# Kernel tuning notes

Measured on AMD Instinct MI355X. Metric: run time of the kernel, lower is better.

The kernel has to match this reference:

```python
import jax, jax.numpy as jnp
import numpy as np

T, B, D_IN = 1024, 64, 17
H_MAIN = 150   # per-direction hidden of main bi-GRU (hidden_dim=300)
H_HIER = 128   # per-direction hidden of hier bi-GRU (hier_hidden=256)
M = 16         # uniform measure length (eoM fires every M steps)
N_MEAS = T // M
N_PITCH, N_KS = 35, 15
PAD_P, PAD_K = 34, 14


def _gru(x, Wih, Whh, bih, bhh):
    # x: [T, N, D]; torch GRU gate order is (r, z, n)
    H = Whh.shape[1]
    gi_all = jnp.einsum('tnd,gd->tng', x, Wih) + bih  # input-side gates, precomputed

    def step(h, gi):
        gh = h @ Whh.T + bhh
        ir, iz, inn = jnp.split(gi, 3, axis=-1)
        hr, hz, hn = jnp.split(gh, 3, axis=-1)
        r = jax.nn.sigmoid(ir + hr)
        z = jax.nn.sigmoid(iz + hz)
        n = jnp.tanh(inn + r * hn)
        h_new = (1.0 - z) * n + z * h
        return h_new, h_new

    h0 = jnp.zeros((x.shape[1], H), x.dtype)
    _, ys = jax.lax.scan(step, h0, gi_all)
    return ys


def _bigru(x, pf, pb):
    yf = _gru(x, *pf)
    yb = _gru(x[::-1], *pb)[::-1]
    return jnp.concatenate([yf, yb], axis=-1)


def _ce(logits, targets, pad_idx):
    # mean cross-entropy with ignore_index=pad_idx
    logp = jax.nn.log_softmax(logits, axis=-1)
    mask = (targets != pad_idx).astype(logits.dtype)
    nll = -jnp.take_along_axis(logp, targets[:, None], axis=1)[:, 0]
    return jnp.sum(nll * mask) / jnp.maximum(jnp.sum(mask), 1.0)


def _forward(sentences, mWih_f, mWhh_f, mbih_f, mbhh_f, mWih_b, mWhh_b, mbih_b, mbhh_b,
             hWih_f, hWhh_f, hbih_f, hbhh_f, hWih_b, hWhh_b, hbih_b, hbhh_b,
             Wq, bq, Wv, bv, Wp, bp, Wk, bk, pitches, keysignatures):
    # main bi-GRU over full sequences: [T, B, 300]
    rnn_out = _bigru(sentences, (mWih_f, mWhh_f, mbih_f, mbhh_f),
                     (mWih_b, mWhh_b, mbih_b, mbhh_b))
    H2 = rnn_out.shape[-1]
    # carve uniform measures: [T,B,H2] -> [M, B*N_MEAS, H2]
    seg = rnn_out.reshape(N_MEAS, M, B, H2).transpose(1, 2, 0, 3).reshape(M, B * N_MEAS, H2)
    hier = _bigru(seg, (hWih_f, hWhh_f, hbih_f, hbhh_f),
                  (hWih_b, hWhh_b, hbih_b, hbhh_b))  # [M, B*N_MEAS, 256]
    HH = hier.shape[-1]
    # attention per measure: query = value = hier outputs [B*N_MEAS, M, 256]
    hv = hier.reshape(M, B, N_MEAS, HH).transpose(1, 2, 0, 3).reshape(B * N_MEAS, M, HH)
    q = hv @ Wq.T + bq
    v = hv @ Wv.T + bv
    attn = jax.nn.softmax(jnp.einsum('nld,nmd->nlm', q, v), axis=-1)
    ctx = jnp.einsum('nlm,nmd->nd', attn, hv).reshape(B, N_MEAS, HH)  # sum over l of attn@value
    # repeat each measure context over its M timesteps: [T, B, 256]
    ctx_t = jnp.repeat(ctx, M, axis=1).transpose(1, 0, 2)
    stacked = jnp.concatenate([rnn_out, ctx_t], axis=-1)  # [T, B, 556]
    out_pitch = stacked @ Wp.T + bp   # [T, B, 35]
    out_ks = ctx_t @ Wk.T + bk        # [T, B, 15]
    return (_ce(out_pitch.reshape(-1, N_PITCH), pitches.reshape(-1), PAD_P)
            + _ce(out_ks.reshape(-1, N_KS), keysignatures.reshape(-1), PAD_K))


def setup_inputs() -> dict:
    key = jax.random.key(0)
    ks = jax.random.split(key, 32)

    def w(i, *shape):
        return jax.random.normal(ks[i], shape, jnp.float32) * 0.05

    G_M, G_H = 3 * H_MAIN, 3 * H_HIER
    inp = {
        'sentences': jax.random.normal(ks[0], (T, B, D_IN), jnp.float32),
        'pitches': jax.random.randint(ks[1], (T, B), 0, PAD_P),
        'keysignatures': jax.random.randint(ks[2], (T, B), 0, PAD_K),
        'sentences_len': jnp.full((B,), T, dtype=jnp.int32),
        'eoM': jnp.tile(((jnp.arange(T) % M) == M - 1).astype(jnp.int32)[:, None], (1, B)),
        'mWih_f': w(3, G_M, D_IN), 'mWhh_f': w(4, G_M, H_MAIN), 'mbih_f': w(5, G_M), 'mbhh_f': w(6, G_M),
        'mWih_b': w(7, G_M, D_IN), 'mWhh_b': w(8, G_M, H_MAIN), 'mbih_b': w(9, G_M), 'mbhh_b': w(10, G_M),
        'hWih_f': w(11, G_H, 2 * H_MAIN), 'hWhh_f': w(12, G_H, H_HIER), 'hbih_f': w(13, G_H), 'hbhh_f': w(14, G_H),
        'hWih_b': w(15, G_H, 2 * H_MAIN), 'hWhh_b': w(16, G_H, H_HIER), 'hbih_b': w(17, G_H), 'hbhh_b': w(18, G_H),
        'Wq': w(19, 2 * H_HIER, 2 * H_HIER), 'bq': w(20, 2 * H_HIER),
        'Wv': w(21, 2 * H_HIER, 2 * H_HIER), 'bv': w(22, 2 * H_HIER),
        'Wp': w(23, N_PITCH, 2 * H_MAIN + 2 * H_HIER), 'bp': w(24, N_PITCH),
        'Wk': w(25, N_KS, 2 * H_HIER), 'bk': w(26, N_KS),
    }
    return inp


def reference(sentences, pitches, keysignatures, sentences_len, eoM,
              mWih_f, mWhh_f, mbih_f, mbhh_f, mWih_b, mWhh_b, mbih_b, mbhh_b,
              hWih_f, hWhh_f, hbih_f, hbhh_f, hWih_b, hWhh_b, hbih_b, hbhh_b,
              Wq, bq, Wv, bv, Wp, bp, Wk, bk):
    # sentences_len/eoM encode the (uniform) measure structure M=16, full lengths;
    # the segment layout is baked in statically, so they are structural constants here.
    return _forward(sentences, mWih_f, mWhh_f, mbih_f, mbhh_f, mWih_b, mWhh_b, mbih_b, mbhh_b,
                    hWih_f, hWhh_f, hbih_f, hbhh_f, hWih_b, hWhh_b, hbih_b, hbhh_b,
                    Wq, bq, Wv, bv, Wp, bp, Wk, bk, pitches, keysignatures)
```

## Files before the change

kernel.cpp:

```cpp
#include <hip/hip_runtime.h>
#include <cstddef>

constexpr int kT   = 1024;
constexpr int kB   = 64;
constexpr int kDIN = 17;
constexpr int kHM  = 150;
constexpr int kHH  = 128;
constexpr int kM   = 16;
constexpr int kD2  = 300;
constexpr int kNP  = 35;
constexpr int kNK  = 15;

constexpr size_t OFF_RNN16  = 0;
constexpr size_t OFF_HV16   = 10485760;
constexpr size_t OFF_HSAVE  = 18874368;
constexpr size_t OFF_PTPACK = 19988480;
constexpr size_t OFF_U      = 20021248;
constexpr size_t OFF_W      = 20021504;
constexpr size_t OFF_C0     = 20021760;
constexpr size_t OFF_ACC    = 20021776;
constexpr size_t OFF_KSLOGP = 20021792;
constexpr size_t OFF_CLOG   = 20083232;
constexpr size_t OFF_BPACK  = 20318752;
constexpr size_t OFF_BPACKL = 20490784;

typedef __bf16 bf16x8 __attribute__((ext_vector_type(8)));
typedef float f32x4 __attribute__((ext_vector_type(4)));

__device__ __forceinline__ unsigned short f2bf(float f) {
  unsigned u = __float_as_uint(f);
  u += 0x7FFFu + ((u >> 16) & 1u);
  return (unsigned short)(u >> 16);
}
__device__ __forceinline__ float bf2f(unsigned short v) {
  return __uint_as_float(((unsigned)v) << 16);
}
__device__ __forceinline__ float sigm(float x) {
  return __builtin_amdgcn_rcpf(1.f + __expf(-x));
}
__device__ __forceinline__ float tanh_fast(float x) {
  return 1.f - 2.f * __builtin_amdgcn_rcpf(__expf(2.f * x) + 1.f);
}

__global__ __launch_bounds__(640, 2) void k_mega(
    const float* __restrict__ x,
    const float* __restrict__ mWih_f, const float* __restrict__ mWhh_f,
    const float* __restrict__ mWih_b, const float* __restrict__ mWhh_b,
    const float* __restrict__ mbih_f, const float* __restrict__ mbhh_f,
    const float* __restrict__ mbih_b, const float* __restrict__ mbhh_b,
    const float* __restrict__ hWih_f, const float* __restrict__ hWhh_f,
    const float* __restrict__ hWih_b, const float* __restrict__ hWhh_b,
    const float* __restrict__ Wp,
    const float* __restrict__ Wq, const float* __restrict__ bq,
    const float* __restrict__ Wv, const float* __restrict__ bv,
    unsigned short* __restrict__ rnn16,
    unsigned short* __restrict__ bpack,
    unsigned short* __restrict__ bpackL,
    unsigned short* __restrict__ pp,
    float* __restrict__ u, float* __restrict__ w,
    float* __restrict__ c0, float* __restrict__ acc,
    float* __restrict__ hsave,
    int t_begin, int t_end)
{
  __shared__ __align__(16) unsigned short hx[2][160];
  __shared__ __align__(16) unsigned short hist[2][16][160];
  __shared__ __align__(16) unsigned short xall[kT][32];
  const int blk = blockIdx.x;
  if (blk < 128) {
    const int d = blk & 1, b = blk >> 1;
    const int tid = threadIdx.x, wv = tid >> 6, lane = tid & 63;
    const int col = lane & 15, q8 = (lane >> 4) * 8;
    for (int i = tid; i < 2 * 160; i += 640) ((unsigned short*)hx)[i] = 0;
    for (int i = tid; i < 2 * 16 * 160; i += 640) ((unsigned short*)hist)[i] = 0;
    {
      const int rlo = d ? (kT - t_end) : t_begin;
      for (int i = tid; i < 512 * 32; i += 640) {
        const int tt = rlo + (i >> 5), c = i & 31;
        xall[tt][c] = (c < kDIN) ? f2bf(x[((size_t)tt * kB + b) * kDIN + c])
                                 : (unsigned short)0;
      }
    }
    const float* bih = d ? mbih_b : mbih_f;
    const float* bhh = d ? mbhh_b : mbhh_f;
    const float* Wihd = d ? mWih_b : mWih_f;
    const float* Whhd = d ? mWhh_b : mWhh_f;
    const int j = wv * 16 + col;
    const bool actv = (lane < 16) && (j < kHM);
    float br = 0.f, bz = 0.f, bnx = 0.f, bnh = 0.f;
    if (actv) {
      br  = bih[j] + bhh[j];
      bz  = bih[150 + j] + bhh[150 + j];
      bnx = bih[300 + j];
      bnh = bhh[300 + j];
    }
    bf16x8 bw[3][6];
    const int gts[3] = { wv, 10 + wv, 20 + wv };
    const int kb = (lane >> 4) * 8;
#pragma unroll
    for (int gi = 0; gi < 3; gi++) {
      const int slot = gts[gi] * 16 + col;
      const int type = slot / 160, jh = slot - type * 160;
      const int row = type * 150 + jh;
      const bool valid = (jh < 150);
#pragma unroll
      for (int kt = 0; kt < 6; kt++) {
        union { bf16x8 v; unsigned short us[8]; } tmp;
        if (kt < 5) {
          const int k0 = kt * 32 + kb;
          if (valid && (k0 + 8 <= 150)) {
#pragma unroll
            for (int p = 0; p < 4; p++) {
              const float2 f2 = *(const float2*)&Whhd[row * 150 + k0 + 2 * p];
              tmp.us[2 * p]     = f2bf(f2.x);
              tmp.us[2 * p + 1] = f2bf(f2.y);
            }
          } else {
#pragma unroll
            for (int jj = 0; jj < 8; jj++) {
              const int k = k0 + jj;
              tmp.us[jj] = (valid && k < 150) ? f2bf(Whhd[row * 150 + k])
                                              : (unsigned short)0;
            }
          }
        } else {
#pragma unroll
          for (int jj = 0; jj < 8; jj++) {
            const int k = kb + jj;
            tmp.us[jj] = (valid && k < 17) ? f2bf(Wihd[row * 17 + k])
                                           : (unsigned short)0;
          }
        }
        bw[gi][kt] = tmp.v;
      }
    }
    float h_old = 0.f;
    if (t_begin > 0 && actv) {
      h_old = hsave[blk * 160 + j];
      hx[t_begin & 1][j] = f2bf(h_old);
    }
    __syncthreads();

    for (int t = t_begin; t < t_end; t++) {
      const int tx = d ? (kT - 1 - t) : t;
      const int buf = t & 1;
      bf16x8 afr[6];
#pragma unroll
      for (int kt = 0; kt < 5; kt++) afr[kt] = *(const bf16x8*)&hx[buf][kt * 32 + q8];
      afr[5] = *(const bf16x8*)&xall[tx][q8];
      f32x4 aR0 = (f32x4)(0.f), aR1 = (f32x4)(0.f);
      f32x4 aZ0 = (f32x4)(0.f), aZ1 = (f32x4)(0.f);
      f32x4 aN0 = (f32x4)(0.f), aN1 = (f32x4)(0.f);
      f32x4 aX  = (f32x4)(0.f);
#pragma unroll
      for (int kt = 0; kt < 6; kt++) {
        const bf16x8 af = afr[kt];
        if ((kt & 1) == 0) {
          aR0 = __builtin_amdgcn_mfma_f32_16x16x32_bf16(af, bw[0][kt], aR0, 0, 0, 0);
          aZ0 = __builtin_amdgcn_mfma_f32_16x16x32_bf16(af, bw[1][kt], aZ0, 0, 0, 0);
          aN0 = __builtin_amdgcn_mfma_f32_16x16x32_bf16(af, bw[2][kt], aN0, 0, 0, 0);
        } else if (kt < 5) {
          aR1 = __builtin_amdgcn_mfma_f32_16x16x32_bf16(af, bw[0][kt], aR1, 0, 0, 0);
          aZ1 = __builtin_amdgcn_mfma_f32_16x16x32_bf16(af, bw[1][kt], aZ1, 0, 0, 0);
          aN1 = __builtin_amdgcn_mfma_f32_16x16x32_bf16(af, bw[2][kt], aN1, 0, 0, 0);
        } else {
          aR1 = __builtin_amdgcn_mfma_f32_16x16x32_bf16(af, bw[0][5], aR1, 0, 0, 0);
          aZ1 = __builtin_amdgcn_mfma_f32_16x16x32_bf16(af, bw[1][5], aZ1, 0, 0, 0);
          aX  = __builtin_amdgcn_mfma_f32_16x16x32_bf16(af, bw[2][5], aX, 0, 0, 0);
        }
      }
      if (actv) {
        const float r = sigm(aR0[0] + aR1[0] + br);
        const float z = sigm(aZ0[0] + aZ1[0] + bz);
        const float n = tanh_fast(aX[0] + bnx + r * (aN0[0] + aN1[0] + bnh));
        h_old = (1.f - z) * n + z * h_old;
        const unsigned short us = f2bf(h_old);
        hx[buf ^ 1][j] = us;
        hist[(t >> 4) & 1][t & 15][j] = us;
      }
      __syncthreads();
      if ((t & 15) == 15) {
        const int hb = (t >> 4) & 1;
        const int toff = tid / 40, ch = tid - toff * 40;
        const int tg = t - 15 + toff;
        const int txg = d ? (kT - 1 - tg) : tg;
        *(ushort4*)&rnn16[((size_t)txg * kB + b) * 320 + d * 160 + ch * 4] =
            *(const ushort4*)&hist[hb][toff][ch * 4];
      }
    }
    if (t_end < kT && actv) hsave[blk * 160 + j] = h_old;
  } else if (blk < 199) {
    const int sub = threadIdx.x >> 6, lane = threadIdx.x & 63;
    int bid = (blk - 128) * 10 + sub;
    if (bid >= 702) return;
    if (bid < 672) {
      const int kt = bid % 14;
      const int nt = (bid / 14) % 24;
      const int d  = bid / (14 * 24);
      const float* Wih = d ? hWih_b : hWih_f;
      const float* Whh = d ? hWhh_b : hWhh_f;
      const int n = nt * 16 + (lane & 15);
      const int kbase = kt * 32 + (lane >> 4) * 8;
      unsigned short* dst = bpack + ((((size_t)d * 24 + nt) * 14 + kt) * 64 + lane) * 8;
#pragma unroll
      for (int jj = 0; jj < 8; jj++) {
        const int k = kbase + jj;
        float f = 0.f;
        if (kt < 10) {
          if (k < 150) f = Wih[n * 300 + k];
          else if (k >= 160 && k < 310) f = Wih[n * 300 + (k - 10)];
        } else {
          f = Whh[n * 128 + (k - 320)];
        }
        dst[jj] = f2bf(f);
      }
    } else {
      bid -= 672;
      const int kt = bid % 10, nt = bid / 10;
      const int n = nt * 16 + (lane & 15);
      const int kbase = kt * 32 + (lane >> 4) * 8;
      unsigned short* dst = bpackL + (((size_t)bid) * 64 + lane) * 8;
#pragma unroll
      for (int jj = 0; jj < 8; jj++) {
        const int k = kbase + jj;
        float f = 0.f;
        if (n < kNP) {
          if (k < 150) f = Wp[n * 556 + k];
          else if (k >= 160 && k < 310) f = Wp[n * 556 + (k - 10)];
        }
        dst[jj] = f2bf(f);
      }
    }
  } else if (blk < 212) {
    const int sub = threadIdx.x >> 6, lane = threadIdx.x & 63;
    const int bid = (blk - 199) * 10 + sub;
    if (bid >= 128) return;
    const int kt = bid & 7, nt = bid >> 3;
    const int c = nt * 16 + (lane & 15);
    const int e0 = kt * 32 + (lane >> 4) * 8;
    float av[8];
#pragma unroll
    for (int jj = 0; jj < 8; jj++) av[jj] = 0.f;
    for (int a = 0; a < 256; a++) {
      const float wq = Wq[a * 256 + c];
#pragma unroll
      for (int jj = 0; jj < 8; jj++) av[jj] += wq * Wv[a * 256 + e0 + jj];
    }
    unsigned short* dst = pp + ((size_t)bid * 64 + lane) * 8;
#pragma unroll
    for (int jj = 0; jj < 8; jj++) dst[jj] = f2bf(av[jj]);
  } else {
    const int a = threadIdx.x;
    if (a >= 256) return;
    float us = 0.f, ws = 0.f;
    for (int jj = 0; jj < 256; jj++) {
      us += Wq[jj * 256 + a] * bv[jj];
      ws += bq[jj] * Wv[jj * 256 + a];
    }
    u[a] = us; w[a] = ws;
    if (a == 0) {
      float cc = 0.f;
      for (int jj = 0; jj < 256; jj++) cc += bq[jj] * bv[jj];
      c0[0] = cc;
      acc[0] = acc[1] = acc[2] = acc[3] = acc[4] = 0.f;
    }
  }
}

__global__ __launch_bounds__(512, 1) void k_hier_mfma(
    const unsigned short* __restrict__ rnn16,
    const unsigned short* __restrict__ bpack,
    const float* __restrict__ bihf, const float* __restrict__ bhhf,
    const float* __restrict__ bihb, const float* __restrict__ bhhb,
    unsigned short* __restrict__ hv16)
{
  const int d = blockIdx.x & 1;
  const int bn0 = (blockIdx.x >> 1) * 16;
  const int tid = threadIdx.x;
  const int w = tid >> 6;
  const int lane = tid & 63;
  const int q = lane >> 4, col = lane & 15, q8 = q * 8;

  __shared__ __align__(16) unsigned short x_s[2][16][328];
  __shared__ __align__(16) unsigned short h_s[16][136];

  for (int i = tid; i < 16 * 136; i += 512) ((unsigned short*)h_s)[i] = 0;
  const float* bih = d ? bihb : bihf;
  const float* bhh = d ? bhhb : bhhf;
  const int j = w * 16 + col;
  const float biR  = bih[j] + bhh[j];
  const float biZ  = bih[128 + j] + bhh[128 + j];
  const float biNX = bih[256 + j];
  const float biNH = bhh[256 + j];
  float h32r[4] = {0.f, 0.f, 0.f, 0.f};

  bf16x8 bw[3][14];
  const unsigned short* bpd = bpack + (size_t)d * 24 * 14 * 64 * 8;
  const int nts[3] = { w, 8 + w, 16 + w };
#pragma unroll
  for (int gi = 0; gi < 3; gi++)
#pragma unroll
    for (int kt = 0; kt < 14; kt++)
      bw[gi][kt] = *(const bf16x8*)&bpd[(((size_t)nts[gi] * 14 + kt) * 64 + lane) * 8];

  const int i0 = tid,        r0 = i0 / 40, c0 = i0 - r0 * 40;
  const int i1 = tid + 512,  r1 = i1 / 40, c1 = i1 - r1 * 40;
  const int bnA = bn0 + r0, bbA = bnA >> 6, nnA = bnA & 63;
  const int bnB = bn0 + r1, bbB = bnB >> 6, nnB = bnB & 63;

  {
    const int mx0 = d ? 15 : 0;
    *(uint4*)&x_s[0][r0][c0 * 8] =
        *(const uint4*)&rnn16[((size_t)(nnA * 16 + mx0) * 64 + bbA) * 320 + c0 * 8];
    if (tid < 128)
      *(uint4*)&x_s[0][r1][c1 * 8] =
          *(const uint4*)&rnn16[((size_t)(nnB * 16 + mx0) * 64 + bbB) * 320 + c1 * 8];
  }
  __syncthreads();

  for (int m = 0; m < kM; m++) {
    const int mx = d ? (15 - m) : m;
    const int buf = m & 1;
    uint4 pf0, pf1;
    const bool has = (m + 1 < kM);
    if (has) {
      const int mxn = d ? (15 - (m + 1)) : (m + 1);
      pf0 = *(const uint4*)&rnn16[((size_t)(nnA * 16 + mxn) * 64 + bbA) * 320 + c0 * 8];
      if (tid < 128)
        pf1 = *(const uint4*)&rnn16[((size_t)(nnB * 16 + mxn) * 64 + bbB) * 320 + c1 * 8];
    }
    f32x4 aR = (f32x4)(0.f), aZ = (f32x4)(0.f), aNX = (f32x4)(0.f), aNH = (f32x4)(0.f);
#pragma unroll
    for (int kt = 0; kt < 14; kt++) {
      const bf16x8 af = (kt < 10) ? *(const bf16x8*)&x_s[buf][col][kt * 32 + q8]
                                  : *(const bf16x8*)&h_s[col][(kt - 10) * 32 + q8];
      aR = __builtin_amdgcn_mfma_f32_16x16x32_bf16(af, bw[0][kt], aR, 0, 0, 0);
      aZ = __builtin_amdgcn_mfma_f32_16x16x32_bf16(af, bw[1][kt], aZ, 0, 0, 0);
      if (kt < 10) aNX = __builtin_amdgcn_mfma_f32_16x16x32_bf16(af, bw[2][kt], aNX, 0, 0, 0);
      else         aNH = __builtin_amdgcn_mfma_f32_16x16x32_bf16(af, bw[2][kt], aNH, 0, 0, 0);
    }
    __syncthreads();
#pragma unroll
    for (int i = 0; i < 4; i++) {
      const int row = q * 4 + i;
      const float rr = sigm(aR[i] + biR);
      const float zz = sigm(aZ[i] + biZ);
      const float nn2 = tanh_fast(aNX[i] + biNX + rr * (aNH[i] + biNH));
      const float hnew = (1.f - zz) * nn2 + zz * h32r[i];
      h32r[i] = hnew;
      const unsigned short us = f2bf(hnew);
      h_s[row][j] = us;
      hv16[((size_t)(bn0 + row) * kM + mx) * 256 + d * kHH + j] = us;
    }
    if (has) {
      *(uint4*)&x_s[buf ^ 1][r0][c0 * 8] = pf0;
      if (tid < 128) *(uint4*)&x_s[buf ^ 1][r1][c1 * 8] = pf1;
    }
    __syncthreads();
  }
}

__global__ __launch_bounds__(256) void k_attn_ctx(
    const unsigned short* __restrict__ hv16, const unsigned short* __restrict__ ptpack,
    const float* __restrict__ u, const float* __restrict__ w,
    const float* __restrict__ c0p,
    const float* __restrict__ Wp, const float* __restrict__ bp,
    const float* __restrict__ Wk, const float* __restrict__ bk,
    float* __restrict__ clog, float* __restrict__ kslogp) {
  const int tid = threadIdx.x;
  const int wv = tid >> 6, lane = tid & 63, col = lane & 15, q = lane >> 4, q8 = q * 8;
  __shared__ __align__(16) unsigned short hv16s[16][264];
  __shared__ __align__(16) unsigned short Ts16[16][264];
  __shared__ __align__(16) float W2[50][260];
  __shared__ __align__(16) float cs[256];
  __shared__ __align__(16) float us[256], wss[256];
  __shared__ float pu[16][17], pw[16][17];
  __shared__ float uh[16], wh[16], SM[16];
  __shared__ float As[16][17];
  __shared__ float arr[64];
  __shared__ float bps[35], bks[15];
  const float c0 = c0p[0];
  for (int i = tid; i < 35 * 256; i += 256) { const int r = i >> 8, c = i & 255; W2[r][c] = Wp[r * 556 + 300 + c]; }
  for (int i = tid; i < 15 * 256; i += 256) { const int r = i >> 8, c = i & 255; W2[35 + r][c] = Wk[r * 256 + c]; }
  us[tid] = u[tid];
  wss[tid] = w[tid];
  if (tid < 35) bps[tid] = bp[tid];
  else if (tid < 50) bks[tid - 35] = bk[tid - 35];
  bf16x8 bpt[4][8];
#pragma unroll
  for (int i2 = 0; i2 < 4; i2++)
#pragma unroll
    for (int kt = 0; kt < 8; kt++)
      bpt[i2][kt] = *(const bf16x8*)&ptpack[((((size_t)(wv * 4 + i2)) * 8 + kt) * 64 + lane) * 8];

  const int srow = tid >> 4, sci = (tid & 15) * 16;
  {
    const unsigned short* src = hv16 + (size_t)(blockIdx.x * 8) * 4096;
#pragma unroll
    for (int k = 0; k < 16; k += 4)
      *(ushort4*)&hv16s[srow][sci + k] = *(const ushort4*)&src[srow * 256 + sci + k];
  }
  __syncthreads();

  for (int ni = 0; ni < 8; ni++) {
    const int n = blockIdx.x * 8 + ni;
    ushort4 pf[4];
    if (ni + 1 < 8) {
      const unsigned short* src = hv16 + (size_t)(n + 1) * 4096;
#pragma unroll
      for (int k2 = 0; k2 < 4; k2++) pf[k2] = *(const ushort4*)&src[srow * 256 + sci + k2 * 4];
    }
    {
      f32x4 acc4[4];
#pragma unroll
      for (int i2 = 0; i2 < 4; i2++) acc4[i2] = (f32x4)(0.f);
#pragma unroll
      for (int kt = 0; kt < 8; kt++) {
        const bf16x8 af = *(const bf16x8*)&hv16s[col][kt * 32 + q8];
#pragma unroll
        for (int i2 = 0; i2 < 4; i2++)
          acc4[i2] = __builtin_amdgcn_mfma_f32_16x16x32_bf16(af, bpt[i2][kt], acc4[i2], 0, 0, 0);
      }
#pragma unroll
      for (int i2 = 0; i2 < 4; i2++) {
        const int nt = wv * 4 + i2;
#pragma unroll
        for (int i = 0; i < 4; i++) Ts16[q * 4 + i][nt * 16 + col] = f2bf(acc4[i2][i]);
      }
    }
    {
      const int l = tid >> 4, s = tid & 15;
      float su = 0.f, sw = 0.f;
#pragma unroll
      for (int a0 = 0; a0 < 16; a0++) {
        const int a = s * 16 + a0;
        const float hvv = bf2f(hv16s[l][a]);
        su += hvv * us[a];
        sw += hvv * wss[a];
      }
      pu[l][s] = su; pw[l][s] = sw;
    }
    __syncthreads();
    if (tid < 16) { float s2 = 0.f; for (int s = 0; s < 16; s++) s2 += pu[tid][s]; uh[tid] = s2; }
    else if (tid < 32) { float s2 = 0.f; for (int s = 0; s < 16; s++) s2 += pw[tid - 16][s]; wh[tid - 16] = s2; }
    __syncthreads();
    if (tid < 64) {
      f32x4 sa = (f32x4)(0.f);
#pragma unroll
      for (int kt = 0; kt < 8; kt++) {
        const bf16x8 af  = *(const bf16x8*)&hv16s[col][kt * 32 + q8];
        const bf16x8 bts = *(const bf16x8*)&Ts16[col][kt * 32 + q8];
        sa = __builtin_amdgcn_mfma_f32_16x16x32_bf16(af, bts, sa, 0, 0, 0);
      }
#pragma unroll
      for (int i = 0; i < 4; i++) {
        const int l = q * 4 + i;
        float sc = sa[i] + c0 + uh[l] + wh[col];
        float mxv = sc;
#pragma unroll
        for (int o = 8; o >= 1; o >>= 1) mxv = fmaxf(mxv, __shfl_xor(mxv, o, 16));
        const float e = __expf(sc - mxv);
        float se = e;
#pragma unroll
        for (int o = 8; o >= 1; o >>= 1) se += __shfl_xor(se, o, 16);
        As[l][col] = e / se;
      }
    }
    __syncthreads();
    if (tid < 16) {
      float s = 0.f;
      for (int l2 = 0; l2 < 16; l2++) s += As[l2][tid];
      SM[tid] = s;
    }
    __syncthreads();
    {
      float cv = 0.f;
#pragma unroll
      for (int m2 = 0; m2 < 16; m2++) cv += SM[m2] * bf2f(hv16s[m2][tid]);
      cs[tid] = cv;
    }
    __syncthreads();
    if (ni + 1 < 8) {
#pragma unroll
      for (int k2 = 0; k2 < 4; k2++) *(ushort4*)&hv16s[srow][sci + k2 * 4] = pf[k2];
    }
    {
      const int o = tid >> 2, s = tid & 3;
      float v = 0.f;
      if (o < 50) {
        for (int k0 = 0; k0 < 64; k0 += 4) {
          const int k = s * 64 + k0;
          const float4 wq = *(const float4*)&W2[o][k];
          const float4 cq = *(const float4*)&cs[k];
          v += wq.x * cq.x + wq.y * cq.y + wq.z * cq.z + wq.w * cq.w;
        }
      }
      v += __shfl_xor(v, 1);
      v += __shfl_xor(v, 2);
      if (o < 50 && s == 0) arr[o] = v;
    }
    __syncthreads();
    if (tid < 35) clog[n * kNP + tid] = arr[tid] + bps[tid];
    if (tid >= 64 && tid < 80) {
      const int t2 = tid - 64;
      float kk = (t2 < 15) ? arr[35 + t2] + bks[t2] : -1e30f;
      float mxv = kk;
#pragma unroll
      for (int off = 8; off >= 1; off >>= 1) mxv = fmaxf(mxv, __shfl_xor(mxv, off, 16));
      const float e = (t2 < 15) ? __expf(kk - mxv) : 0.f;
      float se = e;
#pragma unroll
      for (int off = 8; off >= 1; off >>= 1) se += __shfl_xor(se, off, 16);
      if (t2 < 15) kslogp[n * kNK + t2] = kk - mxv - __logf(se);
    }
    __syncthreads();
  }
}

__global__ __launch_bounds__(256, 2) void k_loss_mfma(
    const unsigned short* __restrict__ rnn16,
    const unsigned short* __restrict__ bpackL,
    const float* __restrict__ clog,
    const float* __restrict__ ks_logp,
    const int* __restrict__ pitches, const int* __restrict__ kss,
    float* __restrict__ acc, float* __restrict__ out) {
  const int tid = threadIdx.x, w = tid >> 6, lane = tid & 63;
  const int col = lane & 15, q = lane >> 4, q8 = q * 8;
  bf16x8 bl[3][10];
#pragma unroll
  for (int nt = 0; nt < 3; nt++)
#pragma unroll
    for (int kt = 0; kt < 10; kt++)
      bl[nt][kt] = *(const bf16x8*)&bpackL[(((size_t)nt * 10 + kt) * 64 + lane) * 8];

  float sp = 0.f, cp = 0.f, sk = 0.f, ck = 0.f;
#pragma unroll
  for (int mt = 0; mt < 2; mt++) {
    const int rowbase = blockIdx.x * 128 + w * 32 + mt * 16;
    f32x4 a0 = (f32x4)(0.f), a1 = (f32x4)(0.f), a2 = (f32x4)(0.f);
#pragma unroll
    for (int kt = 0; kt < 10; kt++) {
      const bf16x8 af = *(const bf16x8*)&rnn16[(size_t)(rowbase + col) * 320 + kt * 32 + q8];
      a0 = __builtin_amdgcn_mfma_f32_16x16x32_bf16(af, bl[0][kt], a0, 0, 0, 0);
      a1 = __builtin_amdgcn_mfma_f32_16x16x32_bf16(af, bl[1][kt], a1, 0, 0, 0);
      a2 = __builtin_amdgcn_mfma_f32_16x16x32_bf16(af, bl[2][kt], a2, 0, 0, 0);
    }
#pragma unroll
    for (int i = 0; i < 4; i++) {
      const int row = rowbase + q * 4 + i;
      const int t = row >> 6, b = row & 63;
      const int bn = b * 64 + (t >> 4);
      const float lg0 = a0[i] + clog[bn * kNP + col];
      const float lg1 = a1[i] + clog[bn * kNP + 16 + col];
      const float lg2 = (col < 3) ? (a2[i] + clog[bn * kNP + 32 + col]) : -1e30f;
      float mx = fmaxf(fmaxf(lg0, lg1), lg2);
#pragma unroll
      for (int o = 8; o >= 1; o >>= 1) mx = fmaxf(mx, __shfl_xor(mx, o, 16));
      float se = __expf(lg0 - mx) + __expf(lg1 - mx) + __expf(lg2 - mx);
#pragma unroll
      for (int o = 8; o >= 1; o >>= 1) se += __shfl_xor(se, o, 16);
      const int tp = pitches[row];
      const float cand = (tp < 16) ? a0[i] : (tp < 32) ? a1[i] : a2[i];
      const float tva = __shfl(cand, (lane & 48) | (tp & 15), 64);
      if (col == 0 && tp != 34) {
        sp += (mx + __logf(se)) - (tva + clog[bn * kNP + tp]);
        cp += 1.f;
      }
      if (col == 1) {
        const int tk = kss[row];
        if (tk != 14) { sk -= ks_logp[bn * kNK + tk]; ck += 1.f; }
      }
    }
  }
#pragma unroll
  for (int o = 32; o >= 1; o >>= 1) {
    sp += __shfl_xor(sp, o, 64);
    cp += __shfl_xor(cp, o, 64);
    sk += __shfl_xor(sk, o, 64);
    ck += __shfl_xor(ck, o, 64);
  }
  if (lane == 0) {
    atomicAdd(&acc[0], sp); atomicAdd(&acc[1], cp);
    atomicAdd(&acc[2], sk); atomicAdd(&acc[3], ck);
  }
  __syncthreads();
  if (tid == 0) {
    __threadfence();
    const float done = atomicAdd(&acc[4], 1.f);
    if (done == (float)(gridDim.x - 1)) {
      const float a0 = atomicAdd(&acc[0], 0.f);
      const float a1 = atomicAdd(&acc[1], 0.f);
      const float a2 = atomicAdd(&acc[2], 0.f);
      const float a3 = atomicAdd(&acc[3], 0.f);
      out[0] = a0 / fmaxf(a1, 1.f) + a2 / fmaxf(a3, 1.f);
    }
  }
}

extern "C" void kernel_launch(void* const* d_in, const int* in_sizes, int n_in,
                              void* d_out, int out_size, void* d_ws, size_t ws_size,
                              hipStream_t stream) {
  (void)in_sizes; (void)n_in; (void)out_size; (void)ws_size;
  const float* sent    = (const float*)d_in[0];
  const int*   pitches = (const int*)d_in[1];
  const int*   kss     = (const int*)d_in[2];
  const float* mWih_f  = (const float*)d_in[5];
  const float* mWhh_f  = (const float*)d_in[6];
  const float* mbih_f  = (const float*)d_in[7];
  const float* mbhh_f  = (const float*)d_in[8];
  const float* mWih_b  = (const float*)d_in[9];
  const float* mWhh_b  = (const float*)d_in[10];
  const float* mbih_b  = (const float*)d_in[11];
  const float* mbhh_b  = (const float*)d_in[12];
  const float* hWih_f  = (const float*)d_in[13];
  const float* hWhh_f  = (const float*)d_in[14];
  const float* hbih_f  = (const float*)d_in[15];
  const float* hbhh_f  = (const float*)d_in[16];
  const float* hWih_b  = (const float*)d_in[17];
  const float* hWhh_b  = (const float*)d_in[18];
  const float* hbih_b  = (const float*)d_in[19];
  const float* hbhh_b  = (const float*)d_in[20];
  const float* Wq      = (const float*)d_in[21];
  const float* bq      = (const float*)d_in[22];
  const float* Wv      = (const float*)d_in[23];
  const float* bv      = (const float*)d_in[24];
  const float* Wp      = (const float*)d_in[25];
  const float* bp      = (const float*)d_in[26];
  const float* Wk      = (const float*)d_in[27];
  const float* bk      = (const float*)d_in[28];
  float* ws  = (float*)d_ws;
  float* out = (float*)d_out;
  unsigned short* rnn16  = (unsigned short*)(ws + OFF_RNN16);
  unsigned short* hv16   = (unsigned short*)(ws + OFF_HV16);
  unsigned short* ptpack = (unsigned short*)(ws + OFF_PTPACK);
  unsigned short* bpackL = (unsigned short*)(ws + OFF_BPACKL);
  unsigned short* bpack  = (unsigned short*)(ws + OFF_BPACK);
  float* hsave = ws + OFF_HSAVE;

  k_mega<<<213, 640, 0, stream>>>(sent,
                                  mWih_f, mWhh_f, mWih_b, mWhh_b,
                                  mbih_f, mbhh_f, mbih_b, mbhh_b,
                                  hWih_f, hWhh_f, hWih_b, hWhh_b, Wp,
                                  Wq, bq, Wv, bv,
                                  rnn16, bpack, bpackL, ptpack,
                                  ws + OFF_U, ws + OFF_W, ws + OFF_C0, ws + OFF_ACC,
                                  hsave, 0, 512);
  k_mega<<<128, 640, 0, stream>>>(sent,
                                  mWih_f, mWhh_f, mWih_b, mWhh_b,
                                  mbih_f, mbhh_f, mbih_b, mbhh_b,
                                  hWih_f, hWhh_f, hWih_b, hWhh_b, Wp,
                                  Wq, bq, Wv, bv,
                                  rnn16, bpack, bpackL, ptpack,
                                  ws + OFF_U, ws + OFF_W, ws + OFF_C0, ws + OFF_ACC,
                                  hsave, 512, 1024);
  k_hier_mfma<<<512, 512, 0, stream>>>(rnn16, bpack,
                                       hbih_f, hbhh_f, hbih_b, hbhh_b, hv16);
  k_attn_ctx<<<512, 256, 0, stream>>>(hv16, ptpack, ws + OFF_U, ws + OFF_W,
                                      ws + OFF_C0, Wp, bp, Wk, bk,
                                      ws + OFF_CLOG, ws + OFF_KSLOGP);
  k_loss_mfma<<<512, 256, 0, stream>>>(rnn16, bpackL, ws + OFF_CLOG, ws + OFF_KSLOGP,
                                       pitches, kss, ws + OFF_ACC, out);
}
```

Measured before the change: 1.026 ms.

## Split main GRU into four phases and stage loss inputs in LDS

The main bi-GRU recurrence now runs as four kernel launches of 256 steps each instead of two of 512. The per-block input tile in shared memory shrinks from 1024 to 256 rows, which cuts LDS use in k_mega and may let more blocks or waves share a CU. Separately, the loss kernel now covers 64 rows per block instead of 128. Each block first copies its rnn16 rows into padded shared memory with 16-byte loads and then feeds the MFMAs from LDS, replacing strided global loads. The cost is two extra launches with hidden-state save and restore, plus an extra sync and LDS traffic in the loss kernel; the remaining unseen part of the loss kernel must also work with the new row mapping.

```diff
diff --git a/kernel.cpp b/kernel.cpp
--- a/kernel.cpp
+++ b/kernel.cpp
@@ -64,7 +64,7 @@
 {
   __shared__ __align__(16) unsigned short hx[2][160];
   __shared__ __align__(16) unsigned short hist[2][16][160];
-  __shared__ __align__(16) unsigned short xall[kT][32];
+  __shared__ __align__(16) unsigned short xall[256][32];
   const int blk = blockIdx.x;
   if (blk < 128) {
     const int d = blk & 1, b = blk >> 1;
@@ -72,13 +72,11 @@
     const int col = lane & 15, q8 = (lane >> 4) * 8;
     for (int i = tid; i < 2 * 160; i += 640) ((unsigned short*)hx)[i] = 0;
     for (int i = tid; i < 2 * 16 * 160; i += 640) ((unsigned short*)hist)[i] = 0;
-    {
-      const int rlo = d ? (kT - t_end) : t_begin;
-      for (int i = tid; i < 512 * 32; i += 640) {
-        const int tt = rlo + (i >> 5), c = i & 31;
-        xall[tt][c] = (c < kDIN) ? f2bf(x[((size_t)tt * kB + b) * kDIN + c])
-                                 : (unsigned short)0;
-      }
+    const int rlo = d ? (kT - t_end) : t_begin;
+    for (int i = tid; i < 256 * 32; i += 640) {
+      const int tt = rlo + (i >> 5), c = i & 31;
+      xall[i >> 5][c] = (c < kDIN) ? f2bf(x[((size_t)tt * kB + b) * kDIN + c])
+                                   : (unsigned short)0;
     }
     const float* bih = d ? mbih_b : mbih_f;
     const float* bhh = d ? mbhh_b : mbhh_f;
@@ -146,7 +144,7 @@
       bf16x8 afr[6];
 #pragma unroll
       for (int kt = 0; kt < 5; kt++) afr[kt] = *(const bf16x8*)&hx[buf][kt * 32 + q8];
-      afr[5] = *(const bf16x8*)&xall[tx][q8];
+      afr[5] = *(const bf16x8*)&xall[tx - rlo][q8];
       f32x4 aR0 = (f32x4)(0.f), aR1 = (f32x4)(0.f);
       f32x4 aZ0 = (f32x4)(0.f), aZ1 = (f32x4)(0.f);
       f32x4 aN0 = (f32x4)(0.f), aN1 = (f32x4)(0.f);
@@ -525,6 +523,7 @@
     float* __restrict__ acc, float* __restrict__ out) {
   const int tid = threadIdx.x, w = tid >> 6, lane = tid & 63;
   const int col = lane & 15, q = lane >> 4, q8 = q * 8;
+  __shared__ __align__(16) unsigned short xls[64][328];
   bf16x8 bl[3][10];
 #pragma unroll
   for (int nt = 0; nt < 3; nt++)
@@ -532,14 +531,22 @@
     for (int kt = 0; kt < 10; kt++)
       bl[nt][kt] = *(const bf16x8*)&bpackL[(((size_t)nt * 10 + kt) * 64 + lane) * 8];
 
+  {
+    const size_t base = (size_t)blockIdx.x * 64;
+    for (int i = tid; i < 64 * 40; i += 256) {
+      const int r = i / 40, c = i - r * 40;
+      *(uint4*)&xls[r][c * 8] = *(const uint4*)&rnn16[(base + r) * 320 + c * 8];
+    }
+  }
+  __syncthreads();
+
   float sp = 0.f, cp = 0.f, sk = 0.f, ck = 0.f;
-#pragma unroll
-  for (int mt = 0; mt < 2; mt++) {
-    const int rowbase = blockIdx.x * 128 + w * 32 + mt * 16;
+  {
+    const int rowbase = blockIdx.x * 64 + w * 16;
     f32x4 a0 = (f32x4)(0.f), a1 = (f32x4)(0.f), a2 = (f32x4)(0.f);
 #pragma unroll
     for (int kt = 0; kt < 10; kt++) {
-      const bf16x8 af = *(const bf16x8*)&rnn16[(size_t)(rowbase + col) * 320 + kt * 32 + q8];
+      const bf16x8 af = *(const bf16x8*)&xls[w * 16 + col][kt * 32 + q8];
       a0 = __builtin_amdgcn_mfma_f32_16x16x32_bf16(af, bl[0][kt], a0, 0, 0, 0);
       a1 = __builtin_amdgcn_mfma_f32_16x16x32_bf16(af, bl[1][kt], a1, 0, 0, 0);
       a2 = __builtin_amdgcn_mfma_f32_16x16x32_bf16(af, bl[2][kt], a2, 0, 0, 0);
@@ -636,27 +643,22 @@
   unsigned short* bpack  = (unsigned short*)(ws + OFF_BPACK);
   float* hsave = ws + OFF_HSAVE;
 
-  k_mega<<<213, 640, 0, stream>>>(sent,
-                                  mWih_f, mWhh_f, mWih_b, mWhh_b,
-                                  mbih_f, mbhh_f, mbih_b, mbhh_b,
-                                  hWih_f, hWhh_f, hWih_b, hWhh_b, Wp,
-                                  Wq, bq, Wv, bv,
-                                  rnn16, bpack, bpackL, ptpack,
-                                  ws + OFF_U, ws + OFF_W, ws + OFF_C0, ws + OFF_ACC,
-                                  hsave, 0, 512);
-  k_mega<<<128, 640, 0, stream>>>(sent,
-                                  mWih_f, mWhh_f, mWih_b, mWhh_b,
-                                  mbih_f, mbhh_f, mbih_b, mbhh_b,
-                                  hWih_f, hWhh_f, hWih_b, hWhh_b, Wp,
-                                  Wq, bq, Wv, bv,
-                                  rnn16, bpack, bpackL, ptpack,
-                                  ws + OFF_U, ws + OFF_W, ws + OFF_C0, ws + OFF_ACC,
-                                  hsave, 512, 1024);
+  for (int ph = 0; ph < 4; ph++) {
+    const int grid = (ph == 0) ? 213 : 128;
+    k_mega<<<grid, 640, 0, stream>>>(sent,
+                                     mWih_f, mWhh_f, mWih_b, mWhh_b,
+                                     mbih_f, mbhh_f, mbih_b, mbhh_b,
+                                     hWih_f, hWhh_f, hWih_b, hWhh_b, Wp,
+                                     Wq, bq, Wv, bv,
+                                     rnn16, bpack, bpackL, ptpack,
+                                     ws + OFF_U, ws + OFF_W, ws + OFF_C0, ws + OFF_ACC,
+                                     hsave, ph * 256, (ph + 1) * 256);
+  }
   k_hier_mfma<<<512, 512, 0, stream>>>(rnn16, bpack,
                                        hbih_f, hbhh_f, hbih_b, hbhh_b, hv16);
   k_attn_ctx<<<512, 256, 0, stream>>>(hv16, ptpack, ws + OFF_U, ws + OFF_W,
                                       ws + OFF_C0, Wp, bp, Wk, bk,
                                       ws + OFF_CLOG, ws + OFF_KSLOGP);
-  k_loss_mfma<<<512, 256, 0, stream>>>(rnn16, bpackL, ws + OFF_CLOG, ws + OFF_KSLOGP,
-                                       pitches, kss, ws + OFF_ACC, out);
-}
+  k_loss_mfma<<<1024, 256, 0, stream>>>(rnn16, bpackL, ws + OFF_CLOG, ws + OFF_KSLOGP,
+                                        pitches, kss, ws + OFF_ACC, out);
+}
```

Result: slower. 1.153 ms (+12.3%).

## Stage loss-kernel rows in LDS, double grid, replace atomics with partial-sum reduction

Applied to the files above, without the earlier changes.

The loss kernel now copies each block's 64 rows of rnn16 into padded shared memory with coalesced 16-byte loads before the MFMA loop, instead of strided per-lane global reads. The grid doubles to 1024 blocks of 64 rows each. Global atomics and the last-block counter are replaced by per-block partial sums written to workspace and a separate one-block final reduction kernel. This adds one extra launch and an LDS staging barrier, and it removes the atomic contention and the accumulator zeroing in k_mega.

```diff
diff --git a/kernel.cpp b/kernel.cpp
--- a/kernel.cpp
+++ b/kernel.cpp
@@ -14,11 +14,11 @@
 constexpr size_t OFF_RNN16  = 0;
 constexpr size_t OFF_HV16   = 10485760;
 constexpr size_t OFF_HSAVE  = 18874368;
+constexpr size_t OFF_PART   = 18894848;
 constexpr size_t OFF_PTPACK = 19988480;
 constexpr size_t OFF_U      = 20021248;
 constexpr size_t OFF_W      = 20021504;
 constexpr size_t OFF_C0     = 20021760;
-constexpr size_t OFF_ACC    = 20021776;
 constexpr size_t OFF_KSLOGP = 20021792;
 constexpr size_t OFF_CLOG   = 20083232;
 constexpr size_t OFF_BPACK  = 20318752;
@@ -58,7 +58,7 @@
     unsigned short* __restrict__ bpackL,
     unsigned short* __restrict__ pp,
     float* __restrict__ u, float* __restrict__ w,
-    float* __restrict__ c0, float* __restrict__ acc,
+    float* __restrict__ c0,
     float* __restrict__ hsave,
     int t_begin, int t_end)
 {
@@ -261,7 +261,6 @@
       float cc = 0.f;
       for (int jj = 0; jj < 256; jj++) cc += bq[jj] * bv[jj];
       c0[0] = cc;
-      acc[0] = acc[1] = acc[2] = acc[3] = acc[4] = 0.f;
     }
   }
 }
@@ -522,9 +521,11 @@
     const float* __restrict__ clog,
     const float* __restrict__ ks_logp,
     const int* __restrict__ pitches, const int* __restrict__ kss,
-    float* __restrict__ acc, float* __restrict__ out) {
+    float4* __restrict__ partial) {
   const int tid = threadIdx.x, w = tid >> 6, lane = tid & 63;
   const int col = lane & 15, q = lane >> 4, q8 = q * 8;
+  __shared__ __align__(16) unsigned short xls[64][328];
+  __shared__ float red[4][4];
   bf16x8 bl[3][10];
 #pragma unroll
   for (int nt = 0; nt < 3; nt++)
@@ -532,14 +533,22 @@
     for (int kt = 0; kt < 10; kt++)
       bl[nt][kt] = *(const bf16x8*)&bpackL[(((size_t)nt * 10 + kt) * 64 + lane) * 8];
 
+  {
+    const size_t base = (size_t)blockIdx.x * 64;
+    for (int i = tid; i < 64 * 40; i += 256) {
+      const int r = i / 40, c = i - r * 40;
+      *(uint4*)&xls[r][c * 8] = *(const uint4*)&rnn16[(base + r) * 320 + c * 8];
+    }
+  }
+  __syncthreads();
+
   float sp = 0.f, cp = 0.f, sk = 0.f, ck = 0.f;
-#pragma unroll
-  for (int mt = 0; mt < 2; mt++) {
-    const int rowbase = blockIdx.x * 128 + w * 32 + mt * 16;
+  {
+    const int rowbase = blockIdx.x * 64 + w * 16;
     f32x4 a0 = (f32x4)(0.f), a1 = (f32x4)(0.f), a2 = (f32x4)(0.f);
 #pragma unroll
     for (int kt = 0; kt < 10; kt++) {
-      const bf16x8 af = *(const bf16x8*)&rnn16[(size_t)(rowbase + col) * 320 + kt * 32 + q8];
+      const bf16x8 af = *(const bf16x8*)&xls[w * 16 + col][kt * 32 + q8];
       a0 = __builtin_amdgcn_mfma_f32_16x16x32_bf16(af, bl[0][kt], a0, 0, 0, 0);
       a1 = __builtin_amdgcn_mfma_f32_16x16x32_bf16(af, bl[1][kt], a1, 0, 0, 0);
       a2 = __builtin_amdgcn_mfma_f32_16x16x32_bf16(af, bl[2][kt], a2, 0, 0, 0);
@@ -578,21 +587,40 @@
     sk += __shfl_xor(sk, o, 64);
     ck += __shfl_xor(ck, o, 64);
   }
-  if (lane == 0) {
-    atomicAdd(&acc[0], sp); atomicAdd(&acc[1], cp);
-    atomicAdd(&acc[2], sk); atomicAdd(&acc[3], ck);
-  }
+  if (lane == 0) { red[w][0] = sp; red[w][1] = cp; red[w][2] = sk; red[w][3] = ck; }
   __syncthreads();
   if (tid == 0) {
-    __threadfence();
-    const float done = atomicAdd(&acc[4], 1.f);
-    if (done == (float)(gridDim.x - 1)) {
-      const float a0 = atomicAdd(&acc[0], 0.f);
-      const float a1 = atomicAdd(&acc[1], 0.f);
-      const float a2 = atomicAdd(&acc[2], 0.f);
-      const float a3 = atomicAdd(&acc[3], 0.f);
-      out[0] = a0 / fmaxf(a1, 1.f) + a2 / fmaxf(a3, 1.f);
-    }
+    float p0 = 0.f, p1 = 0.f, p2 = 0.f, p3 = 0.f;
+#pragma unroll
+    for (int q2 = 0; q2 < 4; q2++) { p0 += red[q2][0]; p1 += red[q2][1]; p2 += red[q2][2]; p3 += red[q2][3]; }
+    partial[blockIdx.x] = make_float4(p0, p1, p2, p3);
+  }
+}
+
+__global__ __launch_bounds__(256) void k_final(const float4* __restrict__ partial,
+                                               float* __restrict__ out) {
+  const int tid = threadIdx.x, w = tid >> 6, lane = tid & 63;
+  __shared__ float4 red[4];
+  float s0 = 0.f, s1 = 0.f, s2 = 0.f, s3 = 0.f;
+#pragma unroll
+  for (int k = 0; k < 4; k++) {
+    const float4 p = partial[tid + 256 * k];
+    s0 += p.x; s1 += p.y; s2 += p.z; s3 += p.w;
+  }
+#pragma unroll
+  for (int o = 32; o >= 1; o >>= 1) {
+    s0 += __shfl_xor(s0, o, 64);
+    s1 += __shfl_xor(s1, o, 64);
+    s2 += __shfl_xor(s2, o, 64);
+    s3 += __shfl_xor(s3, o, 64);
+  }
+  if (lane == 0) red[w] = make_float4(s0, s1, s2, s3);
+  __syncthreads();
+  if (tid == 0) {
+    float a0 = 0.f, a1 = 0.f, a2 = 0.f, a3 = 0.f;
+#pragma unroll
+    for (int q = 0; q < 4; q++) { a0 += red[q].x; a1 += red[q].y; a2 += red[q].z; a3 += red[q].w; }
+    out[0] = a0 / fmaxf(a1, 1.f) + a2 / fmaxf(a3, 1.f);
   }
 }
 
@@ -635,6 +663,7 @@
   unsigned short* bpackL = (unsigned short*)(ws + OFF_BPACKL);
   unsigned short* bpack  = (unsigned short*)(ws + OFF_BPACK);
   float* hsave = ws + OFF_HSAVE;
+  float4* partial = (float4*)(ws + OFF_PART);
 
   k_mega<<<213, 640, 0, stream>>>(sent,
                                   mWih_f, mWhh_f, mWih_b, mWhh_b,
@@ -642,7 +671,7 @@
                                   hWih_f, hWhh_f, hWih_b, hWhh_b, Wp,
                                   Wq, bq, Wv, bv,
                                   rnn16, bpack, bpackL, ptpack,
-                                  ws + OFF_U, ws + OFF_W, ws + OFF_C0, ws + OFF_ACC,
+                                  ws + OFF_U, ws + OFF_W, ws + OFF_C0,
                                   hsave, 0, 512);
   k_mega<<<128, 640, 0, stream>>>(sent,
                                   mWih_f, mWhh_f, mWih_b, mWhh_b,
@@ -650,13 +679,14 @@
                                   hWih_f, hWhh_f, hWih_b, hWhh_b, Wp,
                                   Wq, bq, Wv, bv,
                                   rnn16, bpack, bpackL, ptpack,
-                                  ws + OFF_U, ws + OFF_W, ws + OFF_C0, ws + OFF_ACC,
+                                  ws + OFF_U, ws + OFF_W, ws + OFF_C0,
                                   hsave, 512, 1024);
   k_hier_mfma<<<512, 512, 0, stream>>>(rnn16, bpack,
                                        hbih_f, hbhh_f, hbih_b, hbhh_b, hv16);
   k_attn_ctx<<<512, 256, 0, stream>>>(hv16, ptpack, ws + OFF_U, ws + OFF_W,
                                       ws + OFF_C0, Wp, bp, Wk, bk,
                                       ws + OFF_CLOG, ws + OFF_KSLOGP);
-  k_loss_mfma<<<512, 256, 0, stream>>>(rnn16, bpackL, ws + OFF_CLOG, ws + OFF_KSLOGP,
-                                       pitches, kss, ws + OFF_ACC, out);
-}
+  k_loss_mfma<<<1024, 256, 0, stream>>>(rnn16, bpackL, ws + OFF_CLOG, ws + OFF_KSLOGP,
+                                        pitches, kss, partial);
+  k_final<<<1, 256, 0, stream>>>(partial, out);
+}
```

Measured after the change: 916.2 us. 10.7% less time.
